# Kernel tuning notes

Measured on AMD Instinct MI355X. Metric: run time of the kernel, lower is better.

## Reference

```python
import jax, jax.numpy as jnp
import numpy as np

N_NODES, N_EDGES = 8000, 24000
MUL0_IN, MUL1_IN = 64, 32          # node: 64x0e + 32x1o
MUL0_MSG, MUL1_MSG = 16, 32        # msg:  16x0e + 32x1o
GATE_S, N_GATES = 16, 32           # gate scalars / gates (= mul of 32x1o gated)
RADIAL = 128
EDGE_DIM = 4                       # 1x0e + 1x1o
WNUM = MUL0_IN*MUL0_MSG + MUL0_IN*MUL1_MSG + MUL1_IN*MUL1_MSG + MUL1_IN*MUL0_MSG  # 4608
INV_SQRT3 = 1.0 / np.sqrt(3.0)     # wigner-3j(1,1,0)/(0,1,1)/(1,0,1) magnitude
# e3nn path weights: sqrt(ir_out.dim / sum_paths_into_output(num_elements))
PW_MSG0 = np.sqrt(1.0 / (MUL0_IN + MUL1_IN))                   # tp_msg -> 16x0e
PW_MSG1 = np.sqrt(3.0 / (MUL0_IN + MUL1_IN))                   # tp_msg -> 32x1o
PW_G01 = np.sqrt(1.0 / (MUL0_MSG*MUL0_IN + MUL1_MSG*MUL1_IN))  # FCTP -> 0e outs
PW_G2  = np.sqrt(3.0 / (MUL0_MSG*MUL1_IN + MUL1_MSG*MUL0_IN))  # FCTP -> 1o out
PW_H0 = np.sqrt(1.0 / (GATE_S + MUL1_MSG*MUL1_MSG))            # heavy_tp -> 16x0e
PW_H1 = np.sqrt(3.0 / (GATE_S + GATE_S))                       # heavy_tp -> 32x1o

_trapz = getattr(np, 'trapezoid', np.trapz)
def _cst(f):
    # e3nn normalize2mom constant: 1/sqrt(E_{z~N(0,1)}[f(z)^2])
    xs = np.linspace(-12.0, 12.0, 200001)
    pdf = np.exp(-0.5*xs*xs) / np.sqrt(2.0*np.pi)
    return float(1.0 / np.sqrt(_trapz(f(xs)**2 * pdf, xs)))
CST_SILU = _cst(lambda v: v / (1.0 + np.exp(-v)))
CST_SIG  = _cst(lambda v: 1.0 / (1.0 + np.exp(-v)))
CST_TANH = _cst(np.tanh)


def setup_inputs() -> dict:
    key = jax.random.key(0)
    ks = jax.random.split(key, 19)
    f = lambda k, s: jax.random.normal(k, s, dtype=jnp.float32)
    x = f(ks[0], (N_NODES, MUL0_IN + 3*MUL1_IN))
    edge_attr = f(ks[1], (N_EDGES, EDGE_DIM))
    edge_index = jax.random.randint(ks[2], (2, N_EDGES), 0, N_NODES)
    z = jax.random.randint(ks[3], (N_NODES,), 0, 10)
    canonical = jax.random.randint(ks[4], (N_NODES,), 0, N_NODES)
    W_mlp1 = f(ks[5], (EDGE_DIM, RADIAL))
    W_mlp2 = f(ks[6], (RADIAL, WNUM))
    Wg000 = f(ks[7], (MUL0_MSG, MUL0_IN, GATE_S))
    Wg110 = f(ks[8], (MUL1_MSG, MUL1_IN, GATE_S))
    Wg001 = f(ks[9], (MUL0_MSG, MUL0_IN, N_GATES))
    Wg111 = f(ks[10], (MUL1_MSG, MUL1_IN, N_GATES))
    Wg012 = f(ks[11], (MUL0_MSG, MUL1_IN, MUL1_MSG))
    Wg102 = f(ks[12], (MUL1_MSG, MUL0_IN, MUL1_MSG))
    Wa = f(ks[13], (GATE_S, GATE_S))
    Wb = f(ks[14], (GATE_S, MUL1_MSG))
    Wc = f(ks[15], (MUL1_MSG, GATE_S))
    Wd = f(ks[16], (MUL1_MSG, MUL1_MSG, GATE_S))
    WL0 = f(ks[17], (GATE_S, GATE_S))
    WL1 = f(ks[18], (MUL1_MSG, MUL1_MSG))
    return dict(x=x, edge_attr=edge_attr, W_mlp1=W_mlp1, W_mlp2=W_mlp2,
                Wg000=Wg000, Wg110=Wg110, Wg001=Wg001, Wg111=Wg111,
                Wg012=Wg012, Wg102=Wg102, Wa=Wa, Wb=Wb, Wc=Wc, Wd=Wd,
                WL0=WL0, WL1=WL1, edge_index=edge_index, z=z, canonical=canonical)


def _forward(x, edge_attr, W_mlp1, W_mlp2, Wg000, Wg110, Wg001, Wg111,
             Wg012, Wg102, Wa, Wb, Wc, Wd, WL0, WL1, edge_index, z, canonical):
    N = x.shape[0]
    E = edge_attr.shape[0]
    src, dst = edge_index[0], edge_index[1]
    # ---- radial MLP -> per-edge TP weights (e3nn FullyConnectedNet, normalized silu)
    h = CST_SILU * jax.nn.silu(edge_attr @ (W_mlp1 / np.sqrt(float(EDGE_DIM))))
    w = h @ (W_mlp2 / np.sqrt(float(RADIAL)))                 # (E, 4608)
    s000 = w[:, 0:1024].reshape(E, MUL0_IN, MUL0_MSG)
    s011 = w[:, 1024:3072].reshape(E, MUL0_IN, MUL1_MSG)
    s101 = w[:, 3072:4096].reshape(E, MUL1_IN, MUL1_MSG)
    s110 = w[:, 4096:4608].reshape(E, MUL1_IN, MUL0_MSG)
    # ---- gather source nodes, per-edge equivariant tensor product
    xs0 = x[src, :MUL0_IN]                                    # (E,64)
    xs1 = x[src, MUL0_IN:].reshape(E, MUL1_IN, 3)             # (E,32,3)
    a0 = edge_attr[:, 0]
    a1 = edge_attr[:, 1:4]
    msg0 = PW_MSG0 * (jnp.einsum('e,eu,euw->ew', a0, xs0, s000)
                      + INV_SQRT3 * jnp.einsum('eum,em,euw->ew', xs1, a1, s110))
    msg1 = PW_MSG1 * INV_SQRT3 * (jnp.einsum('eu,em,euw->ewm', xs0, a1, s011)
                                  + jnp.einsum('eum,e,euw->ewm', xs1, a0, s101))
    msg = jnp.concatenate([msg0, msg1.reshape(E, -1)], axis=-1)   # (E,112)
    # ---- scatter_add to destination nodes
    nm = jax.ops.segment_sum(msg, dst, num_segments=N)
    m0 = nm[:, :MUL0_MSG]
    m1 = nm[:, MUL0_MSG:].reshape(N, MUL1_MSG, 3)
    x0 = x[:, :MUL0_IN]
    x1 = x[:, MUL0_IN:].reshape(N, MUL1_IN, 3)
    # ---- FullyConnectedTensorProduct(msg, node) -> scalars | gates | gated
    gs = PW_G01 * (jnp.einsum('nu,nv,uvw->nw', m0, x0, Wg000)
                   + INV_SQRT3 * jnp.einsum('num,nvm,uvw->nw', m1, x1, Wg110))
    gg = PW_G01 * (jnp.einsum('nu,nv,uvw->nw', m0, x0, Wg001)
                   + INV_SQRT3 * jnp.einsum('num,nvm,uvw->nw', m1, x1, Wg111))
    gv = PW_G2 * INV_SQRT3 * (jnp.einsum('nu,nvm,uvw->nwm', m0, x1, Wg012)
                              + jnp.einsum('num,nv,uvw->nwm', m1, x0, Wg102))
    # ---- Gate (normalized sigmoid / tanh)
    xg0 = CST_SIG * jax.nn.sigmoid(gs)                        # (N,16)
    gates = CST_TANH * jnp.tanh(gg)                           # (N,32)
    xg1 = gates[:, :, None] * gv                              # (N,32,3)
    xg = jnp.concatenate([xg0, xg1.reshape(N, -1)], axis=-1)  # (N,112)
    # ---- heavy-atom pooling: scatter_mean of heavy nodes by canonical id
    mask = z > 1
    mf = mask.astype(x.dtype)
    sums = jax.ops.segment_sum(xg * mf[:, None], canonical, num_segments=N)
    cnt = jax.ops.segment_sum(mf, canonical, num_segments=N)
    xh = sums / jnp.maximum(cnt, 1.0)[:, None]
    h0 = xh[:, :GATE_S]
    h1 = xh[:, GATE_S:].reshape(N, MUL1_MSG, 3)
    # ---- heavy self tensor product (internal shared weights)
    t0 = PW_H0 * (jnp.einsum('uv,nu,nv->nu', Wa, h0, h0)
                  + INV_SQRT3 * jnp.einsum('uvw,num,nvm->nw', Wd, h1, h1))
    t1 = PW_H1 * INV_SQRT3 * (jnp.einsum('uv,nu,nvm->nvm', Wb, h0, h1)
                              + jnp.einsum('uv,num,nv->num', Wc, h1, h0))
    th = jnp.concatenate([t0, t1.reshape(N, -1)], axis=-1)
    # ---- broadcast heavy features back to heavy atoms
    y = jnp.where(mask[:, None], th[canonical], xg)
    y0 = y[:, :GATE_S]
    y1 = y[:, GATE_S:].reshape(N, MUL1_MSG, 3)
    # ---- e3nn Linear (per-irrep, 1/sqrt(fan_in))
    out0 = y0 @ (WL0 / np.sqrt(float(GATE_S)))
    out1 = jnp.einsum('num,uw->nwm', y1, WL1) / np.sqrt(float(MUL1_MSG))
    return jnp.concatenate([out0, out1.reshape(N, -1)], axis=-1)  # (N,112)


def reference(x, edge_attr, W_mlp1, W_mlp2, Wg000, Wg110, Wg001, Wg111,
              Wg012, Wg102, Wa, Wb, Wc, Wd, WL0, WL1, edge_index, z, canonical):
    return _forward(x, edge_attr, W_mlp1, W_mlp2, Wg000, Wg110, Wg001, Wg111,
                    Wg012, Wg102, Wa, Wb, Wc, Wd, WL0, WL1, edge_index, z, canonical)
```

## Files before the change

### kernel.cpp

```cpp
#include <hip/hip_runtime.h>
#include <hip/hip_bf16.h>
#include <cmath>


#define N_NODES 8000
#define N_EDGES 24000

#define INV_SQRT3f 0.57735026918962576f
#define PW_MSG0f 0.10206207261596575f
#define PW1f     0.10206207261596575f
#define PW_G01f  0.022097086912079608f
#define PW_G2f   0.034232659844072866f
#define PW_H0f   0.031008683647302115f
#define PW_H1f   0.30618621784789724f
#define RSQRT128f 0.08838834764831845f
#define RSQRT32f  0.17677669529663687f

typedef short short8 __attribute__((ext_vector_type(8)));
typedef short short4v __attribute__((ext_vector_type(4)));
typedef float f32x4 __attribute__((ext_vector_type(4)));

__device__ inline short f32_to_bf16_bits(float v) {
  unsigned int b = __builtin_bit_cast(unsigned int, v);
  b += 0x7fffu + ((b >> 16) & 1u);
  return (short)(b >> 16);
}

__global__ __launch_bounds__(256) void k_prep(const float* __restrict__ W2,
                                              const float* __restrict__ Wg000,
                                              const float* __restrict__ Wg110,
                                              const float* __restrict__ Wg001,
                                              const float* __restrict__ Wg111,
                                              const float* __restrict__ Wg012,
                                              const float* __restrict__ Wg102,
                                              const float* __restrict__ Wd,
                                              const float* __restrict__ WL0,
                                              const float* __restrict__ WL1,
                                              const float* __restrict__ ea,
                                              const float* __restrict__ W1,
                                              short* __restrict__ w2s,
                                              short* __restrict__ bt,
                                              float* __restrict__ wdt,
                                              float* __restrict__ wl0t,
                                              float* __restrict__ wl1t,
                                              short* __restrict__ hbf,
                                              float cst_silu) {
  const int b = blockIdx.x, tid = threadIdx.x;
  if (b < 576) {
    __shared__ float tile[32][33];
    const int kt = b & 3, ct = b >> 2;
    const int k0 = kt*32, c0 = ct*32;
    const int tx = tid & 31, ty = tid >> 5;
#pragma unroll
    for (int i = 0; i < 4; ++i) {
      int r = ty + i*8;
      tile[r][tx] = W2[(k0+r)*4608 + c0 + tx];
    }
    __syncthreads();
#pragma unroll
    for (int i = 0; i < 4; ++i) {
      int r = ty + i*8;
      const int c = c0 + r, k = k0 + tx;
      const int id = (c < 1024) ? (c >> 4)
                   : (c < 4096) ? ((c + 512) >> 4) : ((c - 3072) >> 4);
      const int nn = c & 15, ks = k >> 5, quad = (k >> 3) & 3, jj = k & 7;
      w2s[id*2048 + ks*512 + (quad*16 + nn)*8 + jj] = f32_to_bf16_bits(tile[tx][r]);
    }
  } else if (b < 1344) {
    int i = (b - 576) * 256 + tid;
    float v;
    if (i < 16384) {
      int u = i >> 10, r = i & 1023;
      int ks = r >> 9, lane = (r >> 3) & 63, j = r & 7;
      int k = ks*32 + (lane >> 4)*8 + j, nn = lane & 15;
      v = Wg000[u*1024 + k*16 + nn];
    } else if (i < 49152) {
      int o = i - 16384;
      int tau = o >> 10, r = o & 1023;
      int u = tau >> 1, wh = tau & 1;
      int ks = r >> 9, lane = (r >> 3) & 63, j = r & 7;
      int k = ks*32 + (lane >> 4)*8 + j, nn = lane & 15;
      v = Wg001[u*2048 + k*32 + wh*16 + nn];
    } else if (i < 65536) {
      int o = i - 49152;
      int u = o >> 9, r = o & 511;
      int lane = r >> 3, j = r & 7;
      int k = (lane >> 4)*8 + j, nn = lane & 15;
      v = INV_SQRT3f * Wg110[u*512 + k*16 + nn];
    } else if (i < 98304) {
      int o = i - 65536;
      int tau = o >> 9, r = o & 511;
      int u = tau >> 1, wh = tau & 1;
      int lane = r >> 3, j = r & 7;
      int k = (lane >> 4)*8 + j, nn = lane & 15;
      v = INV_SQRT3f * Wg111[u*1024 + k*32 + wh*16 + nn];
    } else if (i < 131072) {
      int o = i - 98304;
      int tau = o >> 9, r = o & 511;
      int vv = tau >> 1, wh = tau & 1;
      int lane = r >> 3, j = r & 7;
      int k = (lane >> 4)*8 + j, nn = lane & 15;
      v = (k < 16) ? Wg012[k*1024 + vv*32 + wh*16 + nn] : 0.f;
    } else {
      int o = i - 131072;
      int tau = o >> 10, r = o & 1023;
      int u = tau >> 1, wh = tau & 1;
      int ks = r >> 9, lane = (r >> 3) & 63, j = r & 7;
      int k = ks*32 + (lane >> 4)*8 + j, nn = lane & 15;
      v = Wg102[u*2048 + k*32 + wh*16 + nn];
    }
    bt[i] = f32_to_bf16_bits(v);
  } else if (b < 1413) {
    int i = (b - 1344) * 256 + tid;
    if (i < 16384) {
      int k = i >> 10, uv = i & 1023;
      wdt[i] = Wd[uv*16 + k];
    } else if (i < 16640) {
      int j = i - 16384; int jj = j >> 4, v = j & 15;
      wl0t[j] = WL0[v*16 + jj];
    } else if (i < 17664) {
      int j = i - 16640; int w = j >> 5, u = j & 31;
      wl1t[j] = WL1[u*32 + w];
    }
  } else {
    int idx = (b - 1413) * 256 + tid;
    int e = idx >> 5, q = idx & 31;
    const float a0 = ea[e*4+0], a1 = ea[e*4+1], a2 = ea[e*4+2], a3 = ea[e*4+3];
    const float4 w0 = *(const float4*)&W1[q*4];
    const float4 w1 = *(const float4*)&W1[128 + q*4];
    const float4 w2 = *(const float4*)&W1[256 + q*4];
    const float4 w3 = *(const float4*)&W1[384 + q*4];
    float s[4] = {0.5f*(a0*w0.x + a1*w1.x + a2*w2.x + a3*w3.x),
                  0.5f*(a0*w0.y + a1*w1.y + a2*w2.y + a3*w3.y),
                  0.5f*(a0*w0.z + a1*w1.z + a2*w2.z + a3*w3.z),
                  0.5f*(a0*w0.w + a1*w1.w + a2*w2.w + a3*w3.w)};
    short4v o;
#pragma unroll
    for (int i = 0; i < 4; ++i) {
      float sg = 1.f / (1.f + expf(-s[i]));
      o[i] = f32_to_bf16_bits(cst_silu * s[i] * sg * RSQRT128f);
    }
    *(short4v*)&hbf[idx*4] = o;
  }
}

__global__ __launch_bounds__(256, 2) void k2_edge_msg(
    const float* __restrict__ x, const float* __restrict__ ea,
    const short* __restrict__ w2s, const short* __restrict__ hbf,
    const int* __restrict__ ei, float* __restrict__ nm) {
  __shared__ float msg_s[32][116];
  __shared__ float x0pt[64][32];
  __shared__ float z2wt[32][32];
  __shared__ float x1wt[32][32][3];
  __shared__ float a_s[32][4];
  __shared__ int srcs_s[32], dsts_s[32];

  const int tid = threadIdx.x;
  const int e0 = blockIdx.x * 32;

  if (tid < 32) { srcs_s[tid] = ei[e0+tid]; dsts_s[tid] = ei[N_EDGES + e0 + tid]; }
  if (tid < 128) a_s[tid>>2][tid&3] = ea[e0*4 + tid];
  for (int i = tid; i < 32*116; i += 256) (&msg_s[0][0])[i] = 0.f;
  __syncthreads();

  for (int i = tid; i < 2048; i += 256) {
    int e = i >> 6, u = i & 63;
    x0pt[u][e] = PW1f * x[srcs_s[e]*160 + u];
  }
  for (int i = tid; i < 1024; i += 256) {
    int e = i >> 5, u = i & 31;
    const float* xp = &x[srcs_s[e]*160 + 64 + u*3];
    float m0v = xp[0], m1v = xp[1], m2v = xp[2];
    float a0 = a_s[e][0];
    z2wt[u][e] = PW_MSG0f * INV_SQRT3f *
                 (m0v*a_s[e][1] + m1v*a_s[e][2] + m2v*a_s[e][3]);
    x1wt[u][e][0] = PW1f * a0 * m0v;
    x1wt[u][e][1] = PW1f * a0 * m1v;
    x1wt[u][e][2] = PW1f * a0 * m2v;
  }
  __syncthreads();

  const int lane = tid & 63, wv = tid >> 6;
  const int quad = lane >> 4, nn = lane & 15;
  const int eq = quad * 4;

  short8 af[2][4];
#pragma unroll
  for (int t = 0; t < 2; ++t)
#pragma unroll
    for (int ks = 0; ks < 4; ++ks)
      af[t][ks] = *(const short8*)&hbf[(e0 + t*16 + nn)*128 + ks*32 + quad*8];

  float p000[2][4] = {};
  float p0[2][4] = {};
  float p011[2][4] = {};
  float p101[2][4][3] = {};

  short8 B0[4], B1[4], B2[4];
  auto loadB = [&](short8* B, int id) {
    const int idc = (id < 287) ? id : 287;
    const short* p = w2s + idc*2048 + lane*8;
    B[0] = *(const short8*)(p);
    B[1] = *(const short8*)(p + 512);
    B[2] = *(const short8*)(p + 1024);
    B[3] = *(const short8*)(p + 1536);
  };
  auto process = [&](const short8* B, int id) {
    f32x4 c0 = {0.f,0.f,0.f,0.f}, c1 = {0.f,0.f,0.f,0.f};
    c0 = __builtin_amdgcn_mfma_f32_16x16x32_bf16(af[0][0], B[0], c0, 0,0,0);
    c1 = __builtin_amdgcn_mfma_f32_16x16x32_bf16(af[1][0], B[0], c1, 0,0,0);
    c0 = __builtin_amdgcn_mfma_f32_16x16x32_bf16(af[0][1], B[1], c0, 0,0,0);
    c1 = __builtin_amdgcn_mfma_f32_16x16x32_bf16(af[1][1], B[1], c1, 0,0,0);
    c0 = __builtin_amdgcn_mfma_f32_16x16x32_bf16(af[0][2], B[2], c0, 0,0,0);
    c1 = __builtin_amdgcn_mfma_f32_16x16x32_bf16(af[1][2], B[2], c1, 0,0,0);
    c0 = __builtin_amdgcn_mfma_f32_16x16x32_bf16(af[0][3], B[3], c0, 0,0,0);
    c1 = __builtin_amdgcn_mfma_f32_16x16x32_bf16(af[1][3], B[3], c1, 0,0,0);
    if (id < 64) {
      const f32x4 w0 = *(const f32x4*)&x0pt[id][eq];
      const f32x4 w1 = *(const f32x4*)&x0pt[id][16 + eq];
#pragma unroll
      for (int r = 0; r < 4; ++r) { p000[0][r] += w0[r]*c0[r]; p000[1][r] += w1[r]*c1[r]; }
    } else if (id < 96) {
      const int u = id - 64;
      const f32x4 w0 = *(const f32x4*)&z2wt[u][eq];
      const f32x4 w1 = *(const f32x4*)&z2wt[u][16 + eq];
#pragma unroll
      for (int r = 0; r < 4; ++r) { p0[0][r] += w0[r]*c0[r]; p0[1][r] += w1[r]*c1[r]; }
    } else if (id < 224) {
      const int u = (id - 96) >> 1;
      const f32x4 w0 = *(const f32x4*)&x0pt[u][eq];
      const f32x4 w1 = *(const f32x4*)&x0pt[u][16 + eq];
#pragma unroll
      for (int r = 0; r < 4; ++r) { p011[0][r] += w0[r]*c0[r]; p011[1][r] += w1[r]*c1[r]; }
    } else {
      const int u = (id - 224) >> 1;
#pragma unroll
      for (int r = 0; r < 4; ++r) {
        const float* xw0 = &x1wt[u][eq + r][0];
        const float* xw1 = &x1wt[u][16 + eq + r][0];
        p101[0][r][0] += xw0[0]*c0[r]; p101[0][r][1] += xw0[1]*c0[r]; p101[0][r][2] += xw0[2]*c0[r];
        p101[1][r][0] += xw1[0]*c1[r]; p101[1][r][1] += xw1[1]*c1[r]; p101[1][r][2] += xw1[2]*c1[r];
      }
    }
  };

  loadB(B0, wv); loadB(B1, wv + 4);
  int id = wv;
  for (int j = 0; j < 24; ++j) {
    loadB(B2, id + 8);  __builtin_amdgcn_sched_barrier(0); process(B0, id);
    loadB(B0, id + 12); __builtin_amdgcn_sched_barrier(0); process(B1, id + 4);
    loadB(B1, id + 16); __builtin_amdgcn_sched_barrier(0); process(B2, id + 8);
    id += 12;
  }

  const int wcol = (wv & 1)*16 + nn;
#pragma unroll
  for (int t = 0; t < 2; ++t)
#pragma unroll
    for (int r = 0; r < 4; ++r) {
      const int e = t*16 + eq + r;
      atomicAdd(&msg_s[e][nn], a_s[e][0]*p000[t][r] + p0[t][r]);
      const float q = p011[t][r];
      atomicAdd(&msg_s[e][16 + wcol*3 + 0], a_s[e][1]*q + p101[t][r][0]);
      atomicAdd(&msg_s[e][16 + wcol*3 + 1], a_s[e][2]*q + p101[t][r][1]);
      atomicAdd(&msg_s[e][16 + wcol*3 + 2], a_s[e][3]*q + p101[t][r][2]);
    }
  __syncthreads();

  for (int i = tid; i < 32*112; i += 256) {
    int le = i / 112, slot = i - le*112;
    atomicAdd(&nm[dsts_s[le]*112 + slot], msg_s[le][slot]);
  }
}

__global__ __launch_bounds__(256, 2) void k3_gate(const float* __restrict__ x,
                                                  const float* __restrict__ nm,
                                                  const short* __restrict__ bt,
                                                  const int* __restrict__ z,
                                                  const int* __restrict__ canonical,
                                                  float* __restrict__ xg,
                                                  float* __restrict__ sums,
                                                  float* __restrict__ cnt,
                                                  float cst_sig, float cst_tanh) {
  __shared__ short x0b[16][64];
  __shared__ short x1b[3][16][32];
  __shared__ short m0b[16][32];
  __shared__ float m0t[16][16];
  __shared__ float m1t[32][3][16];
  __shared__ float x1t[32][3][16];
  __shared__ float gs_s[16][20];
  __shared__ float gg_s[16][36];
  __shared__ float gv_s[16][100];
  const int tid = threadIdx.x;
  const int n0 = blockIdx.x * 8;

  for (int i = tid; i < 16*160; i += 256) {
    int n = i / 160, f = i - n*160;
    float v = (n < 8) ? x[(n0+n)*160 + f] : 0.f;
    if (f < 64) x0b[n][f] = f32_to_bf16_bits(v);
    else {
      int j = f - 64; int vv = j/3, m = j - vv*3;
      x1b[m][n][vv] = f32_to_bf16_bits(v);
      x1t[vv][m][n] = v;
    }
  }
  for (int i = tid; i < 16*112; i += 256) {
    int n = i / 112, f = i - n*112;
    float v = (n < 8) ? nm[(n0+n)*112 + f] : 0.f;
    if (f < 16) { m0b[n][f] = f32_to_bf16_bits(v); m0t[f][n] = v; }
    else { int j = f - 16; int u = j/3, m = j - u*3; m1t[u][m][n] = v; }
  }
  { int n = tid >> 4, k = tid & 15; m0b[n][16+k] = 0; }
  for (int i = tid; i < 320; i += 256) (&gs_s[0][0])[i] = 0.f;
  for (int i = tid; i < 576; i += 256) (&gg_s[0][0])[i] = 0.f;
  for (int i = tid; i < 1600; i += 256) (&gv_s[0][0])[i] = 0.f;
  __syncthreads();

  const int lane = tid & 63, wv = tid >> 6;
  const int quad = lane >> 4, nn = lane & 15;
  const int eq = quad * 4;
  const int wh = wv & 1, uw = wv >> 1;
  const int l8 = lane * 8;

  const short8 ax0a = *(const short8*)&x0b[nn][quad*8];
  const short8 ax0c = *(const short8*)&x0b[nn][32 + quad*8];
  short8 ax1[3];
#pragma unroll
  for (int m = 0; m < 3; ++m) ax1[m] = *(const short8*)&x1b[m][nn][quad*8];
  const short8 am0 = *(const short8*)&m0b[nn][quad*8];

  const short* b000 = bt;
  const short* b001 = bt + 16384;
  const short* b110 = bt + 49152;
  const short* b111 = bt + 65536;
  const short* b012 = bt + 98304;
  const short* b102 = bt + 131072;

  float gs_p[4] = {}, gg_p[4] = {};
  float gv_p[3][4] = {};

  {
    int u = wv;
    const short* p = b000 + u*1024 + l8;
    short8 ba = *(const short8*)p, bb = *(const short8*)(p + 512);
    for (int i = 0; i < 4; ++i) {
      const int un = (i < 3) ? u + 4 : u;
      const short* np = b000 + un*1024 + l8;
      short8 na = *(const short8*)np, nb = *(const short8*)(np + 512);
      __builtin_amdgcn_sched_barrier(0);
      f32x4 c = {0.f,0.f,0.f,0.f};
      c = __builtin_amdgcn_mfma_f32_16x16x32_bf16(ax0a, ba, c, 0,0,0);
      c = __builtin_amdgcn_mfma_f32_16x16x32_bf16(ax0c, bb, c, 0,0,0);
      const f32x4 t = *(const f32x4*)&m0t[u][eq];
#pragma unroll
      for (int r = 0; r < 4; ++r) gs_p[r] += t[r]*c[r];
      u = un; ba = na; bb = nb;
    }
  }
  {
    int u = wv;
    short8 s0 = *(const short8*)(b110 + u*512 + l8);
    for (int i = 0; i < 8; ++i) {
      const int un = (i < 7) ? u + 4 : u;
      short8 ns = *(const short8*)(b110 + un*512 + l8);
      __builtin_amdgcn_sched_barrier(0);
      f32x4 c0 = {0.f,0.f,0.f,0.f}, c1 = {0.f,0.f,0.f,0.f}, c2 = {0.f,0.f,0.f,0.f};
      c0 = __builtin_amdgcn_mfma_f32_16x16x32_bf16(ax1[0], s0, c0, 0,0,0);
      c1 = __builtin_amdgcn_mfma_f32_16x16x32_bf16(ax1[1], s0, c1, 0,0,0);
      c2 = __builtin_amdgcn_mfma_f32_16x16x32_bf16(ax1[2], s0, c2, 0,0,0);
      const f32x4 t0 = *(const f32x4*)&m1t[u][0][eq];
      const f32x4 t1 = *(const f32x4*)&m1t[u][1][eq];
      const f32x4 t2 = *(const f32x4*)&m1t[u][2][eq];
#pragma unroll
      for (int r = 0; r < 4; ++r) gs_p[r] += t0[r]*c0[r] + t1[r]*c1[r] + t2[r]*c2[r];
      u = un; s0 = ns;
    }
  }
  {
    int u = uw;
    const short* p = b001 + (u*2 + wh)*1024 + l8;
    short8 ba = *(const short8*)p, bb = *(const short8*)(p + 512);
    for (int j = 0; j < 8; ++j) {
      const int un = (j < 7) ? u + 2 : u;
      const short* np = b001 + (un*2 + wh)*1024 + l8;
      short8 na = *(const short8*)np, nb = *(const short8*)(np + 512);
      __builtin_amdgcn_sched_barrier(0);
      f32x4 c = {0.f,0.f,0.f,0.f};
      c = __builtin_amdgcn_mfma_f32_16x16x32_bf16(ax0a, ba, c, 0,0,0);
      c = __builtin_amdgcn_mfma_f32_16x16x32_bf16(ax0c, bb, c, 0,0,0);
      const f32x4 t = *(const f32x4*)&m0t[u][eq];
#pragma unroll
      for (int r = 0; r < 4; ++r) gg_p[r] += t[r]*c[r];
      u = un; ba = na; bb = nb;
    }
  }
  {
    int u = uw;
    short8 s0 = *(const short8*)(b111 + (u*2 + wh)*512 + l8);
    for (int j = 0; j < 16; ++j) {
      const int un = (j < 15) ? u + 2 : u;
      short8 ns = *(const short8*)(b111 + (un*2 + wh)*512 + l8);
      __builtin_amdgcn_sched_barrier(0);
      f32x4 c0 = {0.f,0.f,0.f,0.f}, c1 = {0.f,0.f,0.f,0.f}, c2 = {0.f,0.f,0.f,0.f};
      c0 = __builtin_amdgcn_mfma_f32_16x16x32_bf16(ax1[0], s0, c0, 0,0,0);
      c1 = __builtin_amdgcn_mfma_f32_16x16x32_bf16(ax1[1], s0, c1, 0,0,0);
      c2 = __builtin_amdgcn_mfma_f32_16x16x32_bf16(ax1[2], s0, c2, 0,0,0);
      const f32x4 t0 = *(const f32x4*)&m1t[u][0][eq];
      const f32x4 t1 = *(const f32x4*)&m1t[u][1][eq];
      const f32x4 t2 = *(const f32x4*)&m1t[u][2][eq];
#pragma unroll
      for (int r = 0; r < 4; ++r) gg_p[r] += t0[r]*c0[r] + t1[r]*c1[r] + t2[r]*c2[r];
      u = un; s0 = ns;
    }
  }
  {
    int v = uw;
    short8 s0 = *(const short8*)(b012 + (v*2 + wh)*512 + l8);
    for (int j = 0; j < 16; ++j) {
      const int vn = (j < 15) ? v + 2 : v;
      short8 ns = *(const short8*)(b012 + (vn*2 + wh)*512 + l8);
      __builtin_amdgcn_sched_barrier(0);
      f32x4 c = {0.f,0.f,0.f,0.f};
      c = __builtin_amdgcn_mfma_f32_16x16x32_bf16(am0, s0, c, 0,0,0);
#pragma unroll
      for (int m = 0; m < 3; ++m) {
        const f32x4 t = *(const f32x4*)&x1t[v][m][eq];
#pragma unroll
        for (int r = 0; r < 4; ++r) gv_p[m][r] += t[r]*c[r];
      }
      v = vn; s0 = ns;
    }
  }
  {
    int u = uw;
    const short* p = b102 + (u*2 + wh)*1024 + l8;
    short8 ba = *(const short8*)p, bb = *(const short8*)(p + 512);
    for (int j = 0; j < 16; ++j) {
      const int un = (j < 15) ? u + 2 : u;
      const short* np = b102 + (un*2 + wh)*1024 + l8;
      short8 na = *(const short8*)np, nb = *(const short8*)(np + 512);
      __builtin_amdgcn_sched_barrier(0);
      f32x4 c = {0.f,0.f,0.f,0.f};
      c = __builtin_amdgcn_mfma_f32_16x16x32_bf16(ax0a, ba, c, 0,0,0);
      c = __builtin_amdgcn_mfma_f32_16x16x32_bf16(ax0c, bb, c, 0,0,0);
#pragma unroll
      for (int m = 0; m < 3; ++m) {
        const f32x4 t = *(const f32x4*)&m1t[u][m][eq];
#pragma unroll
        for (int r = 0; r < 4; ++r) gv_p[m][r] += t[r]*c[r];
      }
      u = un; ba = na; bb = nb;
    }
  }

#pragma unroll
  for (int r = 0; r < 4; ++r) {
    atomicAdd(&gs_s[eq + r][nn], gs_p[r]);
    atomicAdd(&gg_s[eq + r][wh*16 + nn], gg_p[r]);
#pragma unroll
    for (int m = 0; m < 3; ++m)
      atomicAdd(&gv_s[eq + r][(wh*16 + nn)*3 + m], gv_p[m][r]);
  }
  __syncthreads();

  for (int i = tid; i < 8*112; i += 256) {
    int n = i / 112, f = i - n*112;
    float o;
    if (f < 16) {
      o = cst_sig / (1.f + expf(-PW_G01f * gs_s[n][f]));
    } else {
      int j = f - 16; int w = j/3;
      float gate = cst_tanh * tanhf(PW_G01f * gg_s[n][w]);
      o = gate * (PW_G2f * INV_SQRT3f) * gv_s[n][j];
    }
    const int gn = n0 + n;
    xg[gn*112 + f] = o;
    if (z[gn] > 1) {
      const int c = canonical[gn];
      atomicAdd(&sums[c*112 + f], o);
      if (f == 0) atomicAdd(&cnt[c], 1.f);
    }
  }
}

__global__ __launch_bounds__(256) void k5_thead(const float* __restrict__ sums,
                                                const float* __restrict__ cnt,
                                                const float* __restrict__ Wa,
                                                const float* __restrict__ Wb,
                                                const float* __restrict__ Wc,
                                                const float* __restrict__ wdt,
                                                float* __restrict__ th) {
  __shared__ float xh_s[4][112];
  __shared__ float cm_s[4][1024];
  __shared__ float red[256];
  const int tid = threadIdx.x;
  const int n0 = blockIdx.x * 4;
  for (int i = tid; i < 4*112; i += 256) {
    int n = i / 112, j = i - n*112;
    float cv = fmaxf(cnt[n0+n], 1.f);
    xh_s[n][j] = sums[(n0+n)*112 + j] / cv;
  }
  __syncthreads();
  for (int i = tid; i < 4096; i += 256) {
    int n = i >> 10, uv = i & 1023, u = uv >> 5, v = uv & 31;
    const float* hh = xh_s[n] + 16;
    cm_s[n][uv] = hh[u*3]*hh[v*3] + hh[u*3+1]*hh[v*3+1] + hh[u*3+2]*hh[v*3+2];
  }
  __syncthreads();
  {
    const int hs = tid >> 6, p = tid & 63;
    const int n = p >> 4, k = p & 15;
    float wd = 0.f;
    const float* cp = cm_s[n] + hs*256;
    const float* wp = wdt + k*1024 + hs*256;
#pragma unroll 4
    for (int uv = 0; uv < 256; uv += 4) {
      const f32x4 a = *(const f32x4*)&cp[uv];
      const f32x4 bq = *(const f32x4*)&wp[uv];
      wd += a[0]*bq[0] + a[1]*bq[1] + a[2]*bq[2] + a[3]*bq[3];
    }
    red[tid] = wd;
  }
  __syncthreads();
  if (tid < 64) {
    int n = tid >> 4, k = tid & 15;
    float sA = 0.f;
    for (int v = 0; v < 16; ++v) sA += Wa[k*16+v]*xh_s[n][v];
    float wd = red[tid] + red[tid + 64] + red[tid + 128] + red[tid + 192];
    th[(n0+n)*112 + k] = PW_H0f*(xh_s[n][k]*sA + INV_SQRT3f*wd);
  }
  if (tid < 128) {
    int n = tid >> 5, j = tid & 31;
    float wb = 0.f, wc = 0.f;
    for (int u = 0; u < 16; ++u) wb += Wb[u*32+j]*xh_s[n][u];
    for (int v = 0; v < 16; ++v) wc += Wc[j*16+v]*xh_s[n][v];
    float cb = PW_H1f * INV_SQRT3f * (wb + wc);
    const float* hh = xh_s[n] + 16;
    float* o = th + (n0+n)*112 + 16 + j*3;
    o[0] = cb*hh[j*3]; o[1] = cb*hh[j*3+1]; o[2] = cb*hh[j*3+2];
  }
}

__global__ __launch_bounds__(256) void k6_out(const float* __restrict__ xg,
                                              const float* __restrict__ th,
                                              const int* __restrict__ z,
                                              const int* __restrict__ canonical,
                                              const float* __restrict__ wl0t,
                                              const float* __restrict__ wl1t,
                                              float* __restrict__ out) {
  int idx = blockIdx.x * 256 + threadIdx.x;
  int n = idx / 112, j = idx - n*112;
  const float* yr = (z[n] > 1) ? (th + canonical[n]*112) : (xg + n*112);
  float o = 0.f;
  if (j < 16) {
    const float* wp = wl0t + j*16;
#pragma unroll 4
    for (int v = 0; v < 16; ++v) o += yr[v]*wp[v];
    o *= 0.25f;
  } else {
    int jj = j - 16, w = jj / 3, m = jj - w*3;
    const float* wp = wl1t + w*32;
#pragma unroll 4
    for (int u = 0; u < 32; ++u) o += yr[16 + u*3 + m]*wp[u];
    o *= RSQRT32f;
  }
  out[idx] = o;
}

namespace {
struct Csts {
  float silu, sig, tanh_;
  Csts() {
    const int NPT = 200001;
    const double a = -12.0, b = 12.0;
    const double dx = (b - a) / (NPT - 1);
    double s1 = 0.0, s2 = 0.0, s3 = 0.0;
    for (int i = 0; i < NPT; ++i) {
      double xv = a + dx*i;
      double pdf = std::exp(-0.5*xv*xv) / std::sqrt(2.0*M_PI);
      double sg = 1.0 / (1.0 + std::exp(-xv));
      double f1 = xv*sg, f2 = sg, f3 = std::tanh(xv);
      double wg = (i == 0 || i == NPT-1) ? 0.5 : 1.0;
      s1 += wg*f1*f1*pdf; s2 += wg*f2*f2*pdf; s3 += wg*f3*f3*pdf;
    }
    silu  = (float)(1.0/std::sqrt(s1*dx));
    sig   = (float)(1.0/std::sqrt(s2*dx));
    tanh_ = (float)(1.0/std::sqrt(s3*dx));
  }
};
}

extern "C" void kernel_launch(void* const* d_in, const int* in_sizes, int n_in,
                              void* d_out, int out_size, void* d_ws, size_t ws_size,
                              hipStream_t stream) {
  const float* x     = (const float*)d_in[0];
  const float* ea    = (const float*)d_in[1];
  const float* W1    = (const float*)d_in[2];
  const float* W2    = (const float*)d_in[3];
  const float* Wg000 = (const float*)d_in[4];
  const float* Wg110 = (const float*)d_in[5];
  const float* Wg001 = (const float*)d_in[6];
  const float* Wg111 = (const float*)d_in[7];
  const float* Wg012 = (const float*)d_in[8];
  const float* Wg102 = (const float*)d_in[9];
  const float* Wa    = (const float*)d_in[10];
  const float* Wb    = (const float*)d_in[11];
  const float* Wc    = (const float*)d_in[12];
  const float* Wd    = (const float*)d_in[13];
  const float* WL0   = (const float*)d_in[14];
  const float* WL1   = (const float*)d_in[15];
  const int* ei      = (const int*)d_in[16];
  const int* z       = (const int*)d_in[17];
  const int* canonical = (const int*)d_in[18];
  float* out = (float*)d_out;

  float* ws   = (float*)d_ws;
  short* hbf  = (short*)ws;
  short* w2s  = (short*)(ws + 1536000);
  short* bt   = (short*)(ws + 1831000);
  float* nm   = ws + 1930000;
  float* sums = ws + 2826000;
  float* cnt  = ws + 3722000;
  float* xg   = ws + 3730000;
  float* th   = ws + 4626000;
  float* wdt  = ws + 5522000;
  float* wl0t = ws + 5538384;
  float* wl1t = ws + 5538640;

  static const Csts C;

  hipMemsetAsync(nm, 0, 1800000*sizeof(float), stream);

  k_prep<<<4413, 256, 0, stream>>>(W2, Wg000, Wg110, Wg001, Wg111, Wg012,
                                   Wg102, Wd, WL0, WL1, ea, W1,
                                   w2s, bt, wdt, wl0t, wl1t, hbf, C.silu);
  k2_edge_msg<<<750, 256, 0, stream>>>(x, ea, w2s, hbf, ei, nm);
  k3_gate<<<1000, 256, 0, stream>>>(x, nm, bt, z, canonical, xg, sums, cnt,
                                    C.sig, C.tanh_);
  k5_thead<<<2000, 256, 0, stream>>>(sums, cnt, Wa, Wb, Wc, wdt, th);
  k6_out<<<3500, 256, 0, stream>>>(xg, th, z, canonical, wl0t, wl1t, out);
}
```

Before: 304.2 us.

## Fold memset into prep kernel and split gate work across block pairs

Removes the separate hipMemsetAsync by having extra k_prep blocks zero the nm/sums/cnt region with vector stores. The gate kernel now processes 16 real nodes per block pair instead of 8 padded-to-16 nodes, with each block of the pair handling half of the output channels and only p==0 doing the scalar-gate paths. This removes the wasted MFMA rows from padding and shortens per-block loops, at the cost of each pair reloading node inputs twice.

```diff
diff --git a/kernel.cpp b/kernel.cpp
--- a/kernel.cpp
+++ b/kernel.cpp
@@ -44,6 +44,7 @@
                                               float* __restrict__ wl0t,
                                               float* __restrict__ wl1t,
                                               short* __restrict__ hbf,
+                                              float* __restrict__ zero_base,
                                               float cst_silu) {
   const int b = blockIdx.x, tid = threadIdx.x;
   if (b < 576) {
@@ -122,7 +123,7 @@
       int j = i - 16640; int w = j >> 5, u = j & 31;
       wl1t[j] = WL1[u*32 + w];
     }
-  } else {
+  } else if (b < 4413) {
     int idx = (b - 1413) * 256 + tid;
     int e = idx >> 5, q = idx & 31;
     const float a0 = ea[e*4+0], a1 = ea[e*4+1], a2 = ea[e*4+2], a3 = ea[e*4+3];
@@ -141,6 +142,12 @@
       o[i] = f32_to_bf16_bits(cst_silu * s[i] * sg * RSQRT128f);
     }
     *(short4v*)&hbf[idx*4] = o;
+  } else {
+    int i = (b - 4413) * 256 + tid;
+    if (i < 450000) {
+      f32x4 zz = {0.f,0.f,0.f,0.f};
+      *(f32x4*)&zero_base[i*4] = zz;
+    }
   }
 }
 
@@ -289,14 +296,16 @@
   __shared__ float m1t[32][3][16];
   __shared__ float x1t[32][3][16];
   __shared__ float gs_s[16][20];
-  __shared__ float gg_s[16][36];
-  __shared__ float gv_s[16][100];
+  __shared__ float gg_s[16][20];
+  __shared__ float gv_s[16][52];
   const int tid = threadIdx.x;
-  const int n0 = blockIdx.x * 8;
+  const int blk = blockIdx.x;
+  const int g = blk >> 1, p = blk & 1;
+  const int n0 = g * 16;
 
   for (int i = tid; i < 16*160; i += 256) {
     int n = i / 160, f = i - n*160;
-    float v = (n < 8) ? x[(n0+n)*160 + f] : 0.f;
+    float v = x[(n0+n)*160 + f];
     if (f < 64) x0b[n][f] = f32_to_bf16_bits(v);
     else {
       int j = f - 64; int vv = j/3, m = j - vv*3;
@@ -306,20 +315,19 @@
   }
   for (int i = tid; i < 16*112; i += 256) {
     int n = i / 112, f = i - n*112;
-    float v = (n < 8) ? nm[(n0+n)*112 + f] : 0.f;
+    float v = nm[(n0+n)*112 + f];
     if (f < 16) { m0b[n][f] = f32_to_bf16_bits(v); m0t[f][n] = v; }
     else { int j = f - 16; int u = j/3, m = j - u*3; m1t[u][m][n] = v; }
   }
   { int n = tid >> 4, k = tid & 15; m0b[n][16+k] = 0; }
   for (int i = tid; i < 320; i += 256) (&gs_s[0][0])[i] = 0.f;
-  for (int i = tid; i < 576; i += 256) (&gg_s[0][0])[i] = 0.f;
-  for (int i = tid; i < 1600; i += 256) (&gv_s[0][0])[i] = 0.f;
+  for (int i = tid; i < 320; i += 256) (&gg_s[0][0])[i] = 0.f;
+  for (int i = tid; i < 832; i += 256) (&gv_s[0][0])[i] = 0.f;
   __syncthreads();
 
   const int lane = tid & 63, wv = tid >> 6;
   const int quad = lane >> 4, nn = lane & 15;
   const int eq = quad * 4;
-  const int wh = wv & 1, uw = wv >> 1;
   const int l8 = lane * 8;
 
   const short8 ax0a = *(const short8*)&x0b[nn][quad*8];
@@ -339,10 +347,10 @@
   float gs_p[4] = {}, gg_p[4] = {};
   float gv_p[3][4] = {};
 
-  {
+  if (p == 0) {
     int u = wv;
-    const short* p = b000 + u*1024 + l8;
-    short8 ba = *(const short8*)p, bb = *(const short8*)(p + 512);
+    const short* pp = b000 + u*1024 + l8;
+    short8 ba = *(const short8*)pp, bb = *(const short8*)(pp + 512);
     for (int i = 0; i < 4; ++i) {
       const int un = (i < 3) ? u + 4 : u;
       const short* np = b000 + un*1024 + l8;
@@ -356,9 +364,7 @@
       for (int r = 0; r < 4; ++r) gs_p[r] += t[r]*c[r];
       u = un; ba = na; bb = nb;
     }
-  }
-  {
-    int u = wv;
+    u = wv;
     short8 s0 = *(const short8*)(b110 + u*512 + l8);
     for (int i = 0; i < 8; ++i) {
       const int un = (i < 7) ? u + 4 : u;
@@ -377,12 +383,12 @@
     }
   }
   {
-    int u = uw;
-    const short* p = b001 + (u*2 + wh)*1024 + l8;
-    short8 ba = *(const short8*)p, bb = *(const short8*)(p + 512);
-    for (int j = 0; j < 8; ++j) {
-      const int un = (j < 7) ? u + 2 : u;
-      const short* np = b001 + (un*2 + wh)*1024 + l8;
+    int u = wv;
+    const short* pp = b001 + (u*2 + p)*1024 + l8;
+    short8 ba = *(const short8*)pp, bb = *(const short8*)(pp + 512);
+    for (int j = 0; j < 4; ++j) {
+      const int un = (j < 3) ? u + 4 : u;
+      const short* np = b001 + (un*2 + p)*1024 + l8;
       short8 na = *(const short8*)np, nb = *(const short8*)(np + 512);
       __builtin_amdgcn_sched_barrier(0);
       f32x4 c = {0.f,0.f,0.f,0.f};
@@ -395,11 +401,11 @@
     }
   }
   {
-    int u = uw;
-    short8 s0 = *(const short8*)(b111 + (u*2 + wh)*512 + l8);
-    for (int j = 0; j < 16; ++j) {
-      const int un = (j < 15) ? u + 2 : u;
-      short8 ns = *(const short8*)(b111 + (un*2 + wh)*512 + l8);
+    int u = wv;
+    short8 s0 = *(const short8*)(b111 + (u*2 + p)*512 + l8);
+    for (int j = 0; j < 8; ++j) {
+      const int un = (j < 7) ? u + 4 : u;
+      short8 ns = *(const short8*)(b111 + (un*2 + p)*512 + l8);
       __builtin_amdgcn_sched_barrier(0);
       f32x4 c0 = {0.f,0.f,0.f,0.f}, c1 = {0.f,0.f,0.f,0.f}, c2 = {0.f,0.f,0.f,0.f};
       c0 = __builtin_amdgcn_mfma_f32_16x16x32_bf16(ax1[0], s0, c0, 0,0,0);
@@ -414,11 +420,11 @@
     }
   }
   {
-    int v = uw;
-    short8 s0 = *(const short8*)(b012 + (v*2 + wh)*512 + l8);
-    for (int j = 0; j < 16; ++j) {
-      const int vn = (j < 15) ? v + 2 : v;
-      short8 ns = *(const short8*)(b012 + (vn*2 + wh)*512 + l8);
+    int v = wv;
+    short8 s0 = *(const short8*)(b012 + (v*2 + p)*512 + l8);
+    for (int j = 0; j < 8; ++j) {
+      const int vn = (j < 7) ? v + 4 : v;
+      short8 ns = *(const short8*)(b012 + (vn*2 + p)*512 + l8);
       __builtin_amdgcn_sched_barrier(0);
       f32x4 c = {0.f,0.f,0.f,0.f};
       c = __builtin_amdgcn_mfma_f32_16x16x32_bf16(am0, s0, c, 0,0,0);
@@ -432,12 +438,12 @@
     }
   }
   {
-    int u = uw;
-    const short* p = b102 + (u*2 + wh)*1024 + l8;
-    short8 ba = *(const short8*)p, bb = *(const short8*)(p + 512);
-    for (int j = 0; j < 16; ++j) {
-      const int un = (j < 15) ? u + 2 : u;
-      const short* np = b102 + (un*2 + wh)*1024 + l8;
+    int u = wv;
+    const short* pp = b102 + (u*2 + p)*1024 + l8;
+    short8 ba = *(const short8*)pp, bb = *(const short8*)(pp + 512);
+    for (int j = 0; j < 8; ++j) {
+      const int un = (j < 7) ? u + 4 : u;
+      const short* np = b102 + (un*2 + p)*1024 + l8;
       short8 na = *(const short8*)np, nb = *(const short8*)(np + 512);
       __builtin_amdgcn_sched_barrier(0);
       f32x4 c = {0.f,0.f,0.f,0.f};
@@ -455,30 +461,35 @@
 
 #pragma unroll
   for (int r = 0; r < 4; ++r) {
-    atomicAdd(&gs_s[eq + r][nn], gs_p[r]);
-    atomicAdd(&gg_s[eq + r][wh*16 + nn], gg_p[r]);
+    if (p == 0) atomicAdd(&gs_s[eq + r][nn], gs_p[r]);
+    atomicAdd(&gg_s[eq + r][nn], gg_p[r]);
 #pragma unroll
     for (int m = 0; m < 3; ++m)
-      atomicAdd(&gv_s[eq + r][(wh*16 + nn)*3 + m], gv_p[m][r]);
-  }
-  __syncthreads();
-
-  for (int i = tid; i < 8*112; i += 256) {
-    int n = i / 112, f = i - n*112;
-    float o;
-    if (f < 16) {
-      o = cst_sig / (1.f + expf(-PW_G01f * gs_s[n][f]));
-    } else {
-      int j = f - 16; int w = j/3;
-      float gate = cst_tanh * tanhf(PW_G01f * gg_s[n][w]);
-      o = gate * (PW_G2f * INV_SQRT3f) * gv_s[n][j];
-    }
+      atomicAdd(&gv_s[eq + r][nn*3 + m], gv_p[m][r]);
+  }
+  __syncthreads();
+
+  for (int i = tid; i < 16*48; i += 256) {
+    int n = i / 48, j = i - n*48;
+    int w = j / 3;
+    float gate = cst_tanh * tanhf(PW_G01f * gg_s[n][w]);
+    float o = gate * (PW_G2f * INV_SQRT3f) * gv_s[n][j];
     const int gn = n0 + n;
+    const int f = 16 + p*48 + j;
     xg[gn*112 + f] = o;
-    if (z[gn] > 1) {
-      const int c = canonical[gn];
-      atomicAdd(&sums[c*112 + f], o);
-      if (f == 0) atomicAdd(&cnt[c], 1.f);
+    if (z[gn] > 1) atomicAdd(&sums[canonical[gn]*112 + f], o);
+  }
+  if (p == 0) {
+    for (int i = tid; i < 16*16; i += 256) {
+      int n = i >> 4, f = i & 15;
+      float o = cst_sig / (1.f + expf(-PW_G01f * gs_s[n][f]));
+      const int gn = n0 + n;
+      xg[gn*112 + f] = o;
+      if (z[gn] > 1) {
+        const int c = canonical[gn];
+        atomicAdd(&sums[c*112 + f], o);
+        if (f == 0) atomicAdd(&cnt[c], 1.f);
+      }
     }
   }
 }
@@ -508,8 +519,8 @@
   }
   __syncthreads();
   {
-    const int hs = tid >> 6, p = tid & 63;
-    const int n = p >> 4, k = p & 15;
+    const int hs = tid >> 6, pq = tid & 63;
+    const int n = pq >> 4, k = pq & 15;
     float wd = 0.f;
     const float* cp = cm_s[n] + hs*256;
     const float* wp = wdt + k*1024 + hs*256;
@@ -629,11 +640,9 @@
 
   static const Csts C;
 
-  hipMemsetAsync(nm, 0, 1800000*sizeof(float), stream);
-
-  k_prep<<<4413, 256, 0, stream>>>(W2, Wg000, Wg110, Wg001, Wg111, Wg012,
+  k_prep<<<6171, 256, 0, stream>>>(W2, Wg000, Wg110, Wg001, Wg111, Wg012,
                                    Wg102, Wd, WL0, WL1, ea, W1,
-                                   w2s, bt, wdt, wl0t, wl1t, hbf, C.silu);
+                                   w2s, bt, wdt, wl0t, wl1t, hbf, nm, C.silu);
   k2_edge_msg<<<750, 256, 0, stream>>>(x, ea, w2s, hbf, ei, nm);
   k3_gate<<<1000, 256, 0, stream>>>(x, nm, bt, z, canonical, xg, sums, cnt,
                                     C.sig, C.tanh_);
```

Result: slower. 471.7 us (+55.1%).
